# Optimization experiments

Measured on AMD Instinct MI355X. Metric: run time of the kernel, lower is better.

## Reference

```python
import jax, jax.numpy as jnp
import numpy as np

B, T, D, H = 4, 2048, 1024, 16
DK, DV, CHUNK = D // H, 2 * D // H, 64  # head_k_dim=64, head_v_dim=128 (expand_v=2.0)
EPS = 1e-5


def setup_inputs() -> dict:
    key = jax.random.key(0)
    ks = jax.random.split(key, 6)
    s = 0.02
    return {
        "x": jax.random.normal(ks[0], (B, T, D), jnp.float32),
        "Wq": jax.random.normal(ks[1], (D, H * DK), jnp.float32) * s,
        "Wk": jax.random.normal(ks[2], (D, H * DK), jnp.float32) * s,
        "Wv": jax.random.normal(ks[3], (D, H * DV), jnp.float32) * s,
        "Wg": jax.random.normal(ks[4], (D, H * DV), jnp.float32) * s,
        "Wo": jax.random.normal(ks[5], (H * DV, D), jnp.float32) * s,
        "g_norm_w": jnp.ones((DV,), jnp.float32),
    }


def _rope(q):
    # q: [B, T, H, DK]; non-interleaved (rotate-half) rotary, base 10000
    half = DK // 2
    inv_freq = 1.0 / (10000.0 ** (jnp.arange(half, dtype=jnp.float32) / half))
    freqs = jnp.arange(T, dtype=jnp.float32)[:, None] * inv_freq  # [T, half]
    cos = jnp.cos(freqs)[None, :, None, :]
    sin = jnp.sin(freqs)[None, :, None, :]
    q1, q2 = q[..., :half], q[..., half:]
    return jnp.concatenate([q1 * cos - q2 * sin, q2 * cos + q1 * sin], axis=-1)


def reference(x, Wq, Wk, Wv, Wg, Wo, g_norm_w):
    q = _rope((x @ Wq).reshape(B, T, H, DK)) * (DK ** -0.5)
    k = _rope((x @ Wk).reshape(B, T, H, DK))
    v = (x @ Wv).reshape(B, T, H, DV)

    N = T // CHUNK
    def tochunks(t):  # [B,T,H,Dh] -> [N,B,H,C,Dh]
        return t.reshape(B, N, CHUNK, H, t.shape[-1]).transpose(1, 0, 3, 2, 4)
    qc, kc, vc = tochunks(q), tochunks(k), tochunks(v)

    # per-head RetNet decay: gamma_h = 1 - 2^{-5-h}
    gamma = 1.0 - jnp.exp2(-5.0 - jnp.arange(H, dtype=jnp.float32))  # [H]
    i = jnp.arange(CHUNK, dtype=jnp.float32)
    # intra-chunk decay mask D[h,i,j] = gamma^{i-j} for j<=i else 0
    Dmask = jnp.where(i[:, None] >= i[None, :],
                      gamma[:, None, None] ** (i[:, None] - i[None, :]), 0.0)  # [H,C,C]
    cross = gamma[:, None] ** (i + 1.0)          # [H,C] query decay vs prev state
    kdec = gamma[:, None] ** (CHUNK - 1.0 - i)   # [H,C] key decay into new state
    chunk_dec = gamma ** CHUNK                   # [H]

    def step(S, qkv):
        q_, k_, v_ = qkv  # [B,H,C,DK], [B,H,C,DK], [B,H,C,DV]
        attn = jnp.einsum('bhid,bhjd->bhij', q_, k_) * Dmask
        o = jnp.einsum('bhij,bhjv->bhiv', attn, v_)
        o = o + jnp.einsum('bhid,bhdv->bhiv', q_ * cross[None, :, :, None], S)
        S = S * chunk_dec[None, :, None, None] + \
            jnp.einsum('bhjd,bhjv->bhdv', k_ * kdec[None, :, :, None], v_)
        return S, o

    S0 = jnp.zeros((B, H, DK, DV), x.dtype)
    _, o = jax.lax.scan(step, S0, (qc, kc, vc))  # [N,B,H,C,DV]
    o = o.transpose(1, 0, 3, 2, 4).reshape(B, T, H, DV)

    # fused RMSNorm + swish gate (FusedRMSNormSwishGate)
    g = (x @ Wg).reshape(B, T, H, DV)
    o = o * jax.lax.rsqrt(jnp.mean(o * o, axis=-1, keepdims=True) + EPS) * g_norm_w
    o = o * (g * jax.nn.sigmoid(g))
    return o.reshape(B, T, H * DV) @ Wo
```

## Files before the change

### kernel.cpp

```cpp
#include <hip/hip_runtime.h>
#include <hip/hip_bf16.h>
#include <math.h>

typedef unsigned short u16;
typedef unsigned int u32;
typedef __attribute__((ext_vector_type(8))) short bf16x8;
typedef __attribute__((ext_vector_type(4))) float f32x4;


__device__ __forceinline__ u16 f2bf(float f) {
  union { float f; unsigned u; } a; a.f = f;
  unsigned u = a.u;
  unsigned r = (u + 0x7fffu + ((u >> 16) & 1u)) >> 16;
  return (u16)r;
}
__device__ __forceinline__ float bf2f(u16 s) {
  union { unsigned u; float f; } a; a.u = ((unsigned)s) << 16; return a.f;
}

__global__ void k_sentinel(float* out) {
  if (threadIdx.x == 0 && blockIdx.x == 0) out[0] = 1.0e6f;
}

__device__ __forceinline__ void split8r(const float* t, bf16x8& hi, bf16x8& lo) {
#pragma unroll
  for (int m = 0; m < 8; ++m) {
    union { float f; u32 u; } c; c.f = t[m];
    union { u32 u; float f; } hf; hf.u = c.u & 0xffff0000u;
    union { float f; u32 u; } lw; lw.f = t[m] - hf.f;
    hi[m] = (short)(u16)(c.u >> 16);
    lo[m] = (short)(u16)(lw.u >> 16);
  }
}
__device__ __forceinline__ void split8p(const float* __restrict__ p, bf16x8& hi, bf16x8& lo) {
  f32x4 a = *(const f32x4*)p;
  f32x4 b = *(const f32x4*)(p + 4);
  float t[8];
  t[0]=a[0]; t[1]=a[1]; t[2]=a[2]; t[3]=a[3]; t[4]=b[0]; t[5]=b[1]; t[6]=b[2]; t[7]=b[3];
  split8r(t, hi, lo);
}

__device__ __forceinline__ void bar_lds() {
  asm volatile("s_waitcnt lgkmcnt(0)" ::: "memory");
  __builtin_amdgcn_sched_barrier(0);
  __builtin_amdgcn_s_barrier();
}

__device__ __forceinline__ void bar_vm() {
  asm volatile("s_waitcnt vmcnt(0)" ::: "memory");
  __builtin_amdgcn_sched_barrier(0);
  __builtin_amdgcn_s_barrier();
}

__device__ __forceinline__ void gload16(const u16* g, u16* l) {
  __builtin_amdgcn_global_load_lds(
      (const __attribute__((address_space(1))) unsigned int*)g,
      (__attribute__((address_space(3))) unsigned int*)l, 16, 0, 0);
}

__global__ __launch_bounds__(256) void k_cvt_x(const float* __restrict__ src, u16* __restrict__ dst) {
  int i = blockIdx.x * 256 + threadIdx.x;
  float4 v = ((const float4*)src)[i];
  ushort4 o;
  o.x = f2bf(v.x); o.y = f2bf(v.y); o.z = f2bf(v.z); o.w = f2bf(v.w);
  ((ushort4*)dst)[i] = o;
}

__global__ __launch_bounds__(256) void k_ropetab(float2* __restrict__ tab) {
  int idx = blockIdx.x * 256 + threadIdx.x;
  int t = idx >> 5, i = idx & 31;
  float invf = powf(10000.f, -(float)i * (1.f / 32.f));
  float ang = (float)t * invf;
  float2 cs; cs.x = cosf(ang); cs.y = sinf(ang);
  tab[idx] = cs;
}

__global__ __launch_bounds__(256) void k_transpose_all(
    const float* __restrict__ Wq, const float* __restrict__ Wk, const float* __restrict__ Wv,
    const float* __restrict__ Wg, const float* __restrict__ Wo,
    u16* __restrict__ Wqkb, u16* __restrict__ Wvgb, u16* __restrict__ Wob) {
  int z = blockIdx.x;
  const float* src; u16* dst; int K, N, bx, by;
  if (z < 1024)      { src = Wq; dst = Wqkb;                       K = 1024; N = 1024; int r = z;        bx = r & 31; by = r >> 5; }
  else if (z < 2048) { src = Wk; dst = Wqkb + (size_t)1024 * 1024; K = 1024; N = 1024; int r = z - 1024; bx = r & 31; by = r >> 5; }
  else if (z < 4096) { src = Wv; dst = Wvgb;                       K = 1024; N = 2048; int r = z - 2048; bx = r & 63; by = r >> 6; }
  else if (z < 6144) { src = Wg; dst = Wvgb + (size_t)2048 * 1024; K = 1024; N = 2048; int r = z - 4096; bx = r & 63; by = r >> 6; }
  else               { src = Wo; dst = Wob;                        K = 2048; N = 1024; int r = z - 6144; bx = r & 31; by = r >> 5; }
  __shared__ float tile[32][33];
  int n0 = bx * 32, k0 = by * 32;
  int tx = threadIdx.x & 31, ty = threadIdx.x >> 5;
  for (int r = 0; r < 32; r += 8)
    tile[ty + r][tx] = src[(size_t)(k0 + ty + r) * N + n0 + tx];
  __syncthreads();
  for (int r = 0; r < 32; r += 8)
    dst[(size_t)(n0 + ty + r) * K + k0 + tx] = f2bf(tile[tx][ty + r]);
}

#define STG64(t, sl)                                                                   \
  {                                                                                    \
    _Pragma("unroll")                                                                  \
    for (int kk = 0; kk < 2; ++kk) {                                                   \
      _Pragma("unroll")                                                                \
      for (int q = 0; q < 2; ++q) {                                                    \
        int s = w * 2 + q;                                                             \
        int dByte = s * 1024 + lane * 16;                                              \
        int u = dByte ^ (((dByte >> 9) & 1) << 5);                                     \
        int row = u >> 6, cb = u & 63;                                                 \
        gload16(&A[(size_t)(i0 + row) * K + (t) * 64 + kk * 32 + (cb >> 1)],           \
                &As[sl][kk][s * 512]);                                                 \
        gload16(&Bt[(size_t)(n0 + row) * K + (t) * 64 + kk * 32 + (cb >> 1)],          \
                &Bs[sl][kk][s * 512]);                                                 \
      }                                                                                \
    }                                                                                  \
  }

__global__ __launch_bounds__(256, 2) void k_gemm_qkvg(const u16* __restrict__ A, const u16* __restrict__ Bt,
                                                      float* __restrict__ qk, u16* __restrict__ vg,
                                                      const float2* __restrict__ tab, int K) {
  __shared__ __attribute__((aligned(16))) u16 As[2][2][128 * 32];
  __shared__ __attribute__((aligned(16))) u16 Bs[2][2][128 * 32];
  int id = blockIdx.y * 48 + blockIdx.x;
  int x = id & 7, loc = id >> 3;
  int bxg = loc / 48, rem = loc - bxg * 48;
  int by8 = rem / 6, bxi = rem - by8 * 6;
  int bx = bxg * 6 + bxi, by = x * 8 + by8;
  int i0 = by * 128, n0 = bx * 128;
  int tid = threadIdx.x;
  int lane = tid & 63, w = tid >> 6;
  int wr = (w >> 1) * 64, wc = (w & 1) * 64;
  f32x4 acc[4][4];
#pragma unroll
  for (int m = 0; m < 4; ++m)
#pragma unroll
    for (int n = 0; n < 4; ++n) acc[m][n] = (f32x4){0.f, 0.f, 0.f, 0.f};
  int fr = lane & 15, kq = lane >> 4;
  int nkt = K >> 6;

  STG64(0, 0);
  bar_vm();
  for (int t = 0; t < nkt; ++t) {
    int sl = t & 1;
    if (t + 1 < nkt) STG64(t + 1, sl ^ 1);
#pragma unroll
    for (int kk = 0; kk < 2; ++kk) {
      bf16x8 af[4], bfr[4];
#pragma unroll
      for (int m = 0; m < 4; ++m) {
        int rr = wr + m * 16 + fr;
        int idx = (rr * 32 + kq * 8) ^ (((rr >> 3) & 1) << 4);
        af[m] = *(const bf16x8*)&As[sl][kk][idx];
      }
#pragma unroll
      for (int n = 0; n < 4; ++n) {
        int rr = wc + n * 16 + fr;
        int idx = (rr * 32 + kq * 8) ^ (((rr >> 3) & 1) << 4);
        bfr[n] = *(const bf16x8*)&Bs[sl][kk][idx];
      }
      __builtin_amdgcn_s_setprio(1);
#pragma unroll
      for (int m = 0; m < 4; ++m)
#pragma unroll
        for (int n = 0; n < 4; ++n)
          acc[m][n] = __builtin_amdgcn_mfma_f32_16x16x32_bf16(af[m], bfr[n], acc[m][n], 0, 0, 0);
      __builtin_amdgcn_s_setprio(0);
    }
    bar_vm();
  }

  int rb = (lane >> 4) * 4, cb2 = lane & 15;
  if (n0 < 2048) {
    float scale = (n0 < 1024) ? 0.125f : 1.0f;
#pragma unroll
    for (int m = 0; m < 4; ++m)
#pragma unroll
      for (int n = 0; n < 2; ++n) {
        int gc = n0 + wc + n * 16 + cb2;
        int ii = n * 16 + cb2;
#pragma unroll
        for (int r = 0; r < 4; ++r) {
          int gr = i0 + wr + m * 16 + rb + r;
          int t = gr & 2047;
          float2 cs = tab[t * 32 + ii];
          float q1 = acc[m][n][r], q2 = acc[m][n + 2][r];
          qk[(size_t)gr * 2048 + gc]      = (q1 * cs.x - q2 * cs.y) * scale;
          qk[(size_t)gr * 2048 + gc + 32] = (q2 * cs.x + q1 * cs.y) * scale;
        }
      }
  } else {
#pragma unroll
    for (int m = 0; m < 4; ++m)
#pragma unroll
      for (int n = 0; n < 4; ++n) {
        int gr = i0 + wr + m * 16 + rb;
        int gc = n0 - 2048 + wc + n * 16 + cb2;
#pragma unroll
        for (int r = 0; r < 4; ++r)
          vg[(size_t)(gr + r) * 4096 + gc] = f2bf(acc[m][n][r]);
      }
  }
}

__global__ __launch_bounds__(256, 2) void k_gemm_out(const u16* __restrict__ A, const u16* __restrict__ Bt,
                                                     float* __restrict__ Cv, int N, int K) {
  __shared__ __attribute__((aligned(16))) u16 As[2][2][128 * 32];
  __shared__ __attribute__((aligned(16))) u16 Bs[2][2][128 * 32];
  int nbx = gridDim.x;
  int id = blockIdx.y * nbx + blockIdx.x;
  int cpx = (nbx * gridDim.y) >> 3;
  int sw = (id & 7) * cpx + (id >> 3);
  int bx = sw % nbx, by = sw / nbx;
  int i0 = by * 128, n0 = bx * 128;
  int tid = threadIdx.x;
  int lane = tid & 63, w = tid >> 6;
  int wr = (w >> 1) * 64, wc = (w & 1) * 64;
  f32x4 acc[4][4];
#pragma unroll
  for (int m = 0; m < 4; ++m)
#pragma unroll
    for (int n = 0; n < 4; ++n) acc[m][n] = (f32x4){0.f, 0.f, 0.f, 0.f};
  int fr = lane & 15, kq = lane >> 4;
  int nkt = K >> 6;

  STG64(0, 0);
  bar_vm();
  for (int t = 0; t < nkt; ++t) {
    int sl = t & 1;
    if (t + 1 < nkt) STG64(t + 1, sl ^ 1);
#pragma unroll
    for (int kk = 0; kk < 2; ++kk) {
      bf16x8 af[4], bfr[4];
#pragma unroll
      for (int m = 0; m < 4; ++m) {
        int rr = wr + m * 16 + fr;
        int idx = (rr * 32 + kq * 8) ^ (((rr >> 3) & 1) << 4);
        af[m] = *(const bf16x8*)&As[sl][kk][idx];
      }
#pragma unroll
      for (int n = 0; n < 4; ++n) {
        int rr = wc + n * 16 + fr;
        int idx = (rr * 32 + kq * 8) ^ (((rr >> 3) & 1) << 4);
        bfr[n] = *(const bf16x8*)&Bs[sl][kk][idx];
      }
      __builtin_amdgcn_s_setprio(1);
#pragma unroll
      for (int m = 0; m < 4; ++m)
#pragma unroll
        for (int n = 0; n < 4; ++n)
          acc[m][n] = __builtin_amdgcn_mfma_f32_16x16x32_bf16(af[m], bfr[n], acc[m][n], 0, 0, 0);
      __builtin_amdgcn_s_setprio(0);
    }
    bar_vm();
  }

  int rb = (lane >> 4) * 4, cb2 = lane & 15;
#pragma unroll
  for (int m = 0; m < 4; ++m)
#pragma unroll
    for (int n = 0; n < 4; ++n) {
      int gr = i0 + wr + m * 16 + rb;
      int gc = n0 + wc + n * 16 + cb2;
#pragma unroll
      for (int r = 0; r < 4; ++r)
        Cv[(size_t)(gr + r) * N + gc] = acc[m][n][r];
    }
}

__global__ __launch_bounds__(512) void k_retention(const float* __restrict__ qk, const u16* __restrict__ vg,
                                                   const float* __restrict__ gnw, u16* __restrict__ og) {
  int bh = blockIdx.x & 63, rq = blockIdx.x >> 6;
  int h = bh & 15, b = bh >> 4;
  int gi0 = rq * 16;

  __shared__ __attribute__((aligned(16))) float qs[16][68];
  __shared__ __attribute__((aligned(16))) float ks[64][68];
  __shared__ __attribute__((aligned(16))) u16 vst[128][88];
  __shared__ __attribute__((aligned(16))) u16 kta_h[8][520];
  __shared__ __attribute__((aligned(16))) u16 kta_l[8][520];
  __shared__ __attribute__((aligned(16))) u16 pa_h[16][68];
  __shared__ __attribute__((aligned(16))) u16 pa_l[16][68];
  __shared__ __attribute__((aligned(16))) u16 sst_h[8][1040];
  __shared__ __attribute__((aligned(16))) u16 sst_l[8][1040];
  __shared__ float dpow[72];
  __shared__ float ssred[8][16];

  int tid = threadIdx.x;
  int w = tid >> 6, l = tid & 63;
  int fr = l & 15, fq = l >> 4;
  float gamma = 1.f - exp2f(-5.f - (float)h);
  if (tid <= 64) dpow[tid] = powf(gamma, (float)tid);
  for (int c = tid; c < 4160; c += 512) { ((u32*)sst_h)[c] = 0; ((u32*)sst_l)[c] = 0; }
  __syncthreads();
  float cdec = dpow[64];

  int e0 = w * 16;
  float gww = gnw[e0 + fr];
  int khmax = (rq < 2) ? 1 : 2;

  int qi = tid >> 4, qd4 = (tid & 15) * 4;
  int sj = tid >> 3, sdg = (tid & 7) * 8;
  int vjp = tid & 31, ve8 = (tid >> 5) * 8;

  f32x4 Sacc[4][2];
#pragma unroll
  for (int dt = 0; dt < 4; ++dt)
#pragma unroll
    for (int nt = 0; nt < 2; ++nt) Sacc[dt][nt] = (f32x4){0.f, 0.f, 0.f, 0.f};

  f32x4 pq = (f32x4){0.f, 0.f, 0.f, 0.f};
  f32x4 pk0, pk1;
  bf16x8 pva, pvb;
  {
    int rowbase = b * 2048;
    if (tid < 256) pq = *(const f32x4*)&qk[(size_t)(rowbase + gi0 + qi) * 2048 + h * 64 + qd4];
    const float* kr = &qk[(size_t)(rowbase + sj) * 2048 + 1024 + h * 64 + sdg];
    pk0 = *(const f32x4*)kr;
    pk1 = *(const f32x4*)(kr + 4);
    const u16* vr = &vg[(size_t)(rowbase + 2 * vjp) * 4096 + h * 128 + ve8];
    pva = *(const bf16x8*)vr;
    pvb = *(const bf16x8*)(vr + 4096);
  }

  for (int n = 0; n < 32; ++n) {
    int rowbase = b * 2048 + n * 64;
    if (tid < 256) *(f32x4*)&qs[qi][qd4] = pq;
    {
      *(f32x4*)&ks[sj][sdg] = pk0;
      *(f32x4*)&ks[sj][sdg + 4] = pk1;
      float kdv = dpow[63 - sj];
      float kd[8];
#pragma unroll
      for (int m = 0; m < 4; ++m) { kd[m] = pk0[m] * kdv; kd[m + 4] = pk1[m] * kdv; }
      bf16x8 kh8, kl8;
      split8r(kd, kh8, kl8);
      int J = sj >> 3, s = sj & 7, dh = tid & 7;
#pragma unroll
      for (int m = 0; m < 8; ++m) {
        int blk = (dh * 8) | (m ^ dh);
        kta_h[J][blk * 8 + s] = (u16)kh8[m];
        kta_l[J][blk * 8 + s] = (u16)kl8[m];
      }
#pragma unroll
      for (int m = 0; m < 8; ++m)
        *(u32*)&vst[ve8 + m][2 * vjp] = (u32)(u16)pva[m] | ((u32)(u16)pvb[m] << 16);
    }
    __syncthreads();
    if (n < 31) {
      int rb2 = rowbase + 64;
      if (tid < 256) pq = *(const f32x4*)&qk[(size_t)(rb2 + gi0 + qi) * 2048 + h * 64 + qd4];
      const float* kr = &qk[(size_t)(rb2 + sj) * 2048 + 1024 + h * 64 + sdg];
      pk0 = *(const f32x4*)kr;
      pk1 = *(const f32x4*)(kr + 4);
      const u16* vr = &vg[(size_t)(rb2 + 2 * vjp) * 4096 + h * 128 + ve8];
      pva = *(const bf16x8*)vr;
      pvb = *(const bf16x8*)(vr + 4096);
    }
    bf16x8 qhc[2], qlc[2];
    split8p(&qs[fr][fq * 8], qhc[0], qlc[0]);
    split8p(&qs[fr][32 + fq * 8], qhc[1], qlc[1]);
    if (w < 4) {
      int ct = w;
      f32x4 at = (f32x4){0.f, 0.f, 0.f, 0.f};
      if (16 * ct <= gi0 + 15) {
#pragma unroll
        for (int kh = 0; kh < 2; ++kh) {
          bf16x8 kbh, kbl;
          split8p(&ks[16 * ct + fr][kh * 32 + fq * 8], kbh, kbl);
          at = __builtin_amdgcn_mfma_f32_16x16x32_bf16(kbh, qhc[kh], at, 0, 0, 0);
          at = __builtin_amdgcn_mfma_f32_16x16x32_bf16(kbl, qhc[kh], at, 0, 0, 0);
          at = __builtin_amdgcn_mfma_f32_16x16x32_bf16(kbh, qlc[kh], at, 0, 0, 0);
        }
      }
      int jb = 16 * ct + fq * 4;
      ushort4 wh, wl;
#pragma unroll
      for (int r = 0; r < 4; ++r) {
        int s = gi0 + fr - (jb + r);
        float val = (s >= 0) ? at[r] * dpow[s] : 0.f;
        union { float f; u32 u; } c; c.f = val;
        union { u32 u; float f; } hf; hf.u = c.u & 0xffff0000u;
        union { float f; u32 u; } lw; lw.f = val - hf.f;
        ((u16*)&wh)[r] = (u16)(c.u >> 16);
        ((u16*)&wl)[r] = (u16)(lw.u >> 16);
      }
      *(ushort4*)&pa_h[fr][jb] = wh;
      *(ushort4*)&pa_l[fr][jb] = wl;
    } else if (n < 31) {
      int eb = (w - 4) * 32;
#pragma unroll
      for (int dt = 0; dt < 4; ++dt)
#pragma unroll
        for (int nt = 0; nt < 2; ++nt)
#pragma unroll
          for (int r = 0; r < 4; ++r) Sacc[dt][nt][r] *= cdec;
      bf16x8 bv[2][2];
#pragma unroll
      for (int kh2 = 0; kh2 < 2; ++kh2)
#pragma unroll
        for (int nt = 0; nt < 2; ++nt)
          bv[kh2][nt] = *(const bf16x8*)&vst[eb + nt * 16 + fr][kh2 * 32 + fq * 8];
#pragma unroll
      for (int kh2 = 0; kh2 < 2; ++kh2) {
#pragma unroll
        for (int dt = 0; dt < 4; ++dt) {
          int d = dt * 16 + fr;
          int blk = d ^ ((dt * 2 + (fr >> 3)) & 7);
          bf16x8 ah = *(const bf16x8*)&kta_h[kh2 * 4 + fq][blk * 8];
          bf16x8 al = *(const bf16x8*)&kta_l[kh2 * 4 + fq][blk * 8];
#pragma unroll
          for (int nt = 0; nt < 2; ++nt) {
            Sacc[dt][nt] = __builtin_amdgcn_mfma_f32_16x16x32_bf16(ah, bv[kh2][nt], Sacc[dt][nt], 0, 0, 0);
            Sacc[dt][nt] = __builtin_amdgcn_mfma_f32_16x16x32_bf16(al, bv[kh2][nt], Sacc[dt][nt], 0, 0, 0);
          }
        }
      }
    }
    bar_lds();
    f32x4 o1 = (f32x4){0.f, 0.f, 0.f, 0.f};
    f32x4 o2 = (f32x4){0.f, 0.f, 0.f, 0.f};
#pragma unroll
    for (int kh2 = 0; kh2 < 2; ++kh2) {
      bf16x8 sh = *(const bf16x8*)&sst_h[kh2 * 4 + fq][(e0 + fr) * 8];
      bf16x8 sl = *(const bf16x8*)&sst_l[kh2 * 4 + fq][(e0 + fr) * 8];
      o2 = __builtin_amdgcn_mfma_f32_16x16x32_bf16(qhc[kh2], sh, o2, 0, 0, 0);
      o2 = __builtin_amdgcn_mfma_f32_16x16x32_bf16(qhc[kh2], sl, o2, 0, 0, 0);
      o2 = __builtin_amdgcn_mfma_f32_16x16x32_bf16(qlc[kh2], sh, o2, 0, 0, 0);
      if (kh2 < khmax) {
        bf16x8 ph = *(const bf16x8*)&pa_h[fr][kh2 * 32 + fq * 8];
        bf16x8 pl = *(const bf16x8*)&pa_l[fr][kh2 * 32 + fq * 8];
        bf16x8 bvv = *(const bf16x8*)&vst[e0 + fr][kh2 * 32 + fq * 8];
        o1 = __builtin_amdgcn_mfma_f32_16x16x32_bf16(ph, bvv, o1, 0, 0, 0);
        o1 = __builtin_amdgcn_mfma_f32_16x16x32_bf16(pl, bvv, o1, 0, 0, 0);
      }
    }
    float ofin[4], ssp[4];
#pragma unroll
    for (int r = 0; r < 4; ++r) {
      int gi = gi0 + fq * 4 + r;
      ofin[r] = o1[r] + dpow[gi + 1] * o2[r];
      ssp[r] = ofin[r] * ofin[r];
    }
#pragma unroll
    for (int r = 0; r < 4; ++r) {
      ssp[r] += __shfl_xor(ssp[r], 1, 64);
      ssp[r] += __shfl_xor(ssp[r], 2, 64);
      ssp[r] += __shfl_xor(ssp[r], 4, 64);
      ssp[r] += __shfl_xor(ssp[r], 8, 64);
    }
    if (fr == 0) {
#pragma unroll
      for (int r = 0; r < 4; ++r) ssred[w][fq * 4 + r] = ssp[r];
    }
    bar_lds();
#pragma unroll
    for (int r = 0; r < 4; ++r) {
      int i16 = fq * 4 + r;
      float tot = 0.f;
#pragma unroll
      for (int w2 = 0; w2 < 8; ++w2) tot += ssred[w2][i16];
      float rms = rsqrtf(tot * (1.f / 128.f) + 1e-5f);
      int grow = rowbase + gi0 + i16;
      float g = bf2f(vg[(size_t)grow * 4096 + 2048 + h * 128 + e0 + fr]);
      float y = ofin[r] * rms * gww * (g / (1.f + expf(-g)));
      og[(size_t)grow * 2048 + h * 128 + e0 + fr] = f2bf(y);
    }
    if (w >= 4 && n < 31) {
      int eb = (w - 4) * 32;
#pragma unroll
      for (int dt = 0; dt < 4; ++dt) {
        int g = dt * 2 + (fq >> 1);
#pragma unroll
        for (int nt = 0; nt < 2; ++nt) {
          int e = eb + nt * 16 + fr;
          ushort4 wh, wl;
#pragma unroll
          for (int r = 0; r < 4; ++r) {
            union { float f; u32 u; } c; c.f = Sacc[dt][nt][r];
            union { u32 u; float f; } hf; hf.u = c.u & 0xffff0000u;
            union { float f; u32 u; } lw; lw.f = Sacc[dt][nt][r] - hf.f;
            ((u16*)&wh)[r] = (u16)(c.u >> 16);
            ((u16*)&wl)[r] = (u16)(lw.u >> 16);
          }
          int idx = e * 8 + (fq & 1) * 4;
          *(ushort4*)&sst_h[g][idx] = wh;
          *(ushort4*)&sst_l[g][idx] = wl;
        }
      }
    }
  }
}

extern "C" void kernel_launch(void* const* d_in, const int* in_sizes, int n_in,
                              void* d_out, int out_size, void* d_ws, size_t ws_size,
                              hipStream_t stream) {
  const float* x   = (const float*)d_in[0];
  const float* Wq  = (const float*)d_in[1];
  const float* Wk  = (const float*)d_in[2];
  const float* Wv  = (const float*)d_in[3];
  const float* Wg  = (const float*)d_in[4];
  const float* Wo  = (const float*)d_in[5];
  const float* gnw = (const float*)d_in[6];
  float* out = (float*)d_out;

  const size_t MB = 1024 * 1024;
  char* ws = (char*)d_ws;
  u16*   xb   = (u16*)(ws + 0 * MB);
  u16*   Wqkb = (u16*)(ws + 16 * MB);
  u16*   Wvgb = (u16*)(ws + 20 * MB);
  float2* tab = (float2*)(ws + 28 * MB);
  float* qk   = (float*)(ws + 32 * MB);
  u16*   vg   = (u16*)(ws + 96 * MB);
  u16*   Wob  = (u16*)(ws + 160 * MB);
  u16*   og   = (u16*)(ws + 0 * MB);
  const size_t NEED = 164 * MB;
  if (ws_size < NEED) {
    k_sentinel<<<1, 64, 0, stream>>>(out);
    return;
  }

  k_cvt_x<<<8192, 256, 0, stream>>>(x, xb);
  k_ropetab<<<256, 256, 0, stream>>>(tab);
  k_transpose_all<<<8192, 256, 0, stream>>>(Wq, Wk, Wv, Wg, Wo, Wqkb, Wvgb, Wob);

  k_gemm_qkvg<<<dim3(48, 64), 256, 0, stream>>>(xb, Wqkb, qk, vg, tab, 1024);
  k_retention<<<256, 512, 0, stream>>>(qk, vg, gnw, og);
  k_gemm_out<<<dim3(8, 64), 256, 0, stream>>>(og, Wob, out, 1024, 2048);
}
```

Baseline: 288.9 us.

## Enlarge GEMM tiles to 256x128 with K-step 32 in both projection GEMMs

Measured after the change: 310.1 us. +7.3%, slower.

```diff
diff --git a/kernel.cpp b/kernel.cpp
--- a/kernel.cpp
+++ b/kernel.cpp
@@ -96,74 +96,73 @@
     dst[(size_t)(n0 + ty + r) * K + k0 + tx] = f2bf(tile[tx][ty + r]);
 }
 
-#define STG64(t, sl)                                                                   \
-  {                                                                                    \
-    _Pragma("unroll")                                                                  \
-    for (int kk = 0; kk < 2; ++kk) {                                                   \
-      _Pragma("unroll")                                                                \
-      for (int q = 0; q < 2; ++q) {                                                    \
-        int s = w * 2 + q;                                                             \
-        int dByte = s * 1024 + lane * 16;                                              \
-        int u = dByte ^ (((dByte >> 9) & 1) << 5);                                     \
-        int row = u >> 6, cb = u & 63;                                                 \
-        gload16(&A[(size_t)(i0 + row) * K + (t) * 64 + kk * 32 + (cb >> 1)],           \
-                &As[sl][kk][s * 512]);                                                 \
-        gload16(&Bt[(size_t)(n0 + row) * K + (t) * 64 + kk * 32 + (cb >> 1)],          \
-                &Bs[sl][kk][s * 512]);                                                 \
-      }                                                                                \
-    }                                                                                  \
+#define STG(t, sl)                                                                  \
+  {                                                                                 \
+    _Pragma("unroll")                                                               \
+    for (int q = 0; q < 4; ++q) {                                                   \
+      int s = w * 4 + q;                                                            \
+      int dByte = s * 1024 + lane * 16;                                             \
+      int u = dByte ^ (((dByte >> 9) & 1) << 5);                                    \
+      int row = u >> 6, cb = u & 63;                                                \
+      gload16(&A[(size_t)(i0 + row) * K + (t) * 32 + (cb >> 1)], &As[sl][s * 512]); \
+    }                                                                               \
+    _Pragma("unroll")                                                               \
+    for (int q = 0; q < 2; ++q) {                                                   \
+      int s = w * 2 + q;                                                            \
+      int dByte = s * 1024 + lane * 16;                                             \
+      int u = dByte ^ (((dByte >> 9) & 1) << 5);                                    \
+      int row = u >> 6, cb = u & 63;                                                \
+      gload16(&Bt[(size_t)(n0 + row) * K + (t) * 32 + (cb >> 1)], &Bs[sl][s * 512]);\
+    }                                                                               \
   }
 
 __global__ __launch_bounds__(256, 2) void k_gemm_qkvg(const u16* __restrict__ A, const u16* __restrict__ Bt,
                                                       float* __restrict__ qk, u16* __restrict__ vg,
                                                       const float2* __restrict__ tab, int K) {
-  __shared__ __attribute__((aligned(16))) u16 As[2][2][128 * 32];
-  __shared__ __attribute__((aligned(16))) u16 Bs[2][2][128 * 32];
-  int id = blockIdx.y * 48 + blockIdx.x;
-  int x = id & 7, loc = id >> 3;
-  int bxg = loc / 48, rem = loc - bxg * 48;
-  int by8 = rem / 6, bxi = rem - by8 * 6;
-  int bx = bxg * 6 + bxi, by = x * 8 + by8;
-  int i0 = by * 128, n0 = bx * 128;
+  __shared__ __attribute__((aligned(16))) u16 As[2][256 * 32];
+  __shared__ __attribute__((aligned(16))) u16 Bs[2][128 * 32];
+  int nbx = gridDim.x;
+  int id = blockIdx.y * nbx + blockIdx.x;
+  int cpx = (nbx * gridDim.y) >> 3;
+  int sw = (id & 7) * cpx + (id >> 3);
+  int bx = sw % nbx, by = sw / nbx;
+  int i0 = by * 256, n0 = bx * 128;
   int tid = threadIdx.x;
   int lane = tid & 63, w = tid >> 6;
-  int wr = (w >> 1) * 64, wc = (w & 1) * 64;
-  f32x4 acc[4][4];
-#pragma unroll
-  for (int m = 0; m < 4; ++m)
+  int wr = (w >> 1) * 128, wc = (w & 1) * 64;
+  f32x4 acc[8][4];
+#pragma unroll
+  for (int m = 0; m < 8; ++m)
 #pragma unroll
     for (int n = 0; n < 4; ++n) acc[m][n] = (f32x4){0.f, 0.f, 0.f, 0.f};
   int fr = lane & 15, kq = lane >> 4;
-  int nkt = K >> 6;
-
-  STG64(0, 0);
+  int nkt = K >> 5;
+
+  STG(0, 0);
   bar_vm();
   for (int t = 0; t < nkt; ++t) {
     int sl = t & 1;
-    if (t + 1 < nkt) STG64(t + 1, sl ^ 1);
-#pragma unroll
-    for (int kk = 0; kk < 2; ++kk) {
-      bf16x8 af[4], bfr[4];
-#pragma unroll
-      for (int m = 0; m < 4; ++m) {
-        int rr = wr + m * 16 + fr;
-        int idx = (rr * 32 + kq * 8) ^ (((rr >> 3) & 1) << 4);
-        af[m] = *(const bf16x8*)&As[sl][kk][idx];
-      }
-#pragma unroll
-      for (int n = 0; n < 4; ++n) {
-        int rr = wc + n * 16 + fr;
-        int idx = (rr * 32 + kq * 8) ^ (((rr >> 3) & 1) << 4);
-        bfr[n] = *(const bf16x8*)&Bs[sl][kk][idx];
-      }
-      __builtin_amdgcn_s_setprio(1);
-#pragma unroll
-      for (int m = 0; m < 4; ++m)
-#pragma unroll
-        for (int n = 0; n < 4; ++n)
-          acc[m][n] = __builtin_amdgcn_mfma_f32_16x16x32_bf16(af[m], bfr[n], acc[m][n], 0, 0, 0);
-      __builtin_amdgcn_s_setprio(0);
-    }
+    if (t + 1 < nkt) STG(t + 1, sl ^ 1);
+    bf16x8 af[8], bfr[4];
+#pragma unroll
+    for (int m = 0; m < 8; ++m) {
+      int rr = wr + m * 16 + fr;
+      int idx = (rr * 32 + kq * 8) ^ (((rr >> 3) & 1) << 4);
+      af[m] = *(const bf16x8*)&As[sl][idx];
+    }
+#pragma unroll
+    for (int n = 0; n < 4; ++n) {
+      int rr = wc + n * 16 + fr;
+      int idx = (rr * 32 + kq * 8) ^ (((rr >> 3) & 1) << 4);
+      bfr[n] = *(const bf16x8*)&Bs[sl][idx];
+    }
+    __builtin_amdgcn_s_setprio(1);
+#pragma unroll
+    for (int m = 0; m < 8; ++m)
+#pragma unroll
+      for (int n = 0; n < 4; ++n)
+        acc[m][n] = __builtin_amdgcn_mfma_f32_16x16x32_bf16(af[m], bfr[n], acc[m][n], 0, 0, 0);
+    __builtin_amdgcn_s_setprio(0);
     bar_vm();
   }
 
@@ -171,7 +170,7 @@
   if (n0 < 2048) {
     float scale = (n0 < 1024) ? 0.125f : 1.0f;
 #pragma unroll
-    for (int m = 0; m < 4; ++m)
+    for (int m = 0; m < 8; ++m)
 #pragma unroll
       for (int n = 0; n < 2; ++n) {
         int gc = n0 + wc + n * 16 + cb2;
@@ -188,7 +187,7 @@
       }
   } else {
 #pragma unroll
-    for (int m = 0; m < 4; ++m)
+    for (int m = 0; m < 8; ++m)
 #pragma unroll
       for (int n = 0; n < 4; ++n) {
         int gr = i0 + wr + m * 16 + rb;
@@ -202,59 +201,56 @@
 
 __global__ __launch_bounds__(256, 2) void k_gemm_out(const u16* __restrict__ A, const u16* __restrict__ Bt,
                                                      float* __restrict__ Cv, int N, int K) {
-  __shared__ __attribute__((aligned(16))) u16 As[2][2][128 * 32];
-  __shared__ __attribute__((aligned(16))) u16 Bs[2][2][128 * 32];
+  __shared__ __attribute__((aligned(16))) u16 As[2][256 * 32];
+  __shared__ __attribute__((aligned(16))) u16 Bs[2][128 * 32];
   int nbx = gridDim.x;
   int id = blockIdx.y * nbx + blockIdx.x;
   int cpx = (nbx * gridDim.y) >> 3;
   int sw = (id & 7) * cpx + (id >> 3);
   int bx = sw % nbx, by = sw / nbx;
-  int i0 = by * 128, n0 = bx * 128;
+  int i0 = by * 256, n0 = bx * 128;
   int tid = threadIdx.x;
   int lane = tid & 63, w = tid >> 6;
-  int wr = (w >> 1) * 64, wc = (w & 1) * 64;
-  f32x4 acc[4][4];
-#pragma unroll
-  for (int m = 0; m < 4; ++m)
+  int wr = (w >> 1) * 128, wc = (w & 1) * 64;
+  f32x4 acc[8][4];
+#pragma unroll
+  for (int m = 0; m < 8; ++m)
 #pragma unroll
     for (int n = 0; n < 4; ++n) acc[m][n] = (f32x4){0.f, 0.f, 0.f, 0.f};
   int fr = lane & 15, kq = lane >> 4;
-  int nkt = K >> 6;
-
-  STG64(0, 0);
+  int nkt = K >> 5;
+
+  STG(0, 0);
   bar_vm();
   for (int t = 0; t < nkt; ++t) {
     int sl = t & 1;
-    if (t + 1 < nkt) STG64(t + 1, sl ^ 1);
-#pragma unroll
-    for (int kk = 0; kk < 2; ++kk) {
-      bf16x8 af[4], bfr[4];
-#pragma unroll
-      for (int m = 0; m < 4; ++m) {
-        int rr = wr + m * 16 + fr;
-        int idx = (rr * 32 + kq * 8) ^ (((rr >> 3) & 1) << 4);
-        af[m] = *(const bf16x8*)&As[sl][kk][idx];
-      }
-#pragma unroll
-      for (int n = 0; n < 4; ++n) {
-        int rr = wc + n * 16 + fr;
-        int idx = (rr * 32 + kq * 8) ^ (((rr >> 3) & 1) << 4);
-        bfr[n] = *(const bf16x8*)&Bs[sl][kk][idx];
-      }
-      __builtin_amdgcn_s_setprio(1);
-#pragma unroll
-      for (int m = 0; m < 4; ++m)
-#pragma unroll
-        for (int n = 0; n < 4; ++n)
-          acc[m][n] = __builtin_amdgcn_mfma_f32_16x16x32_bf16(af[m], bfr[n], acc[m][n], 0, 0, 0);
-      __builtin_amdgcn_s_setprio(0);
-    }
+    if (t + 1 < nkt) STG(t + 1, sl ^ 1);
+    bf16x8 af[8], bfr[4];
+#pragma unroll
+    for (int m = 0; m < 8; ++m) {
+      int rr = wr + m * 16 + fr;
+      int idx = (rr * 32 + kq * 8) ^ (((rr >> 3) & 1) << 4);
+      af[m] = *(const bf16x8*)&As[sl][idx];
+    }
+#pragma unroll
+    for (int n = 0; n < 4; ++n) {
+      int rr = wc + n * 16 + fr;
+      int idx = (rr * 32 + kq * 8) ^ (((rr >> 3) & 1) << 4);
+      bfr[n] = *(const bf16x8*)&Bs[sl][idx];
+    }
+    __builtin_amdgcn_s_setprio(1);
+#pragma unroll
+    for (int m = 0; m < 8; ++m)
+#pragma unroll
+      for (int n = 0; n < 4; ++n)
+        acc[m][n] = __builtin_amdgcn_mfma_f32_16x16x32_bf16(af[m], bfr[n], acc[m][n], 0, 0, 0);
+    __builtin_amdgcn_s_setprio(0);
     bar_vm();
   }
 
   int rb = (lane >> 4) * 4, cb2 = lane & 15;
 #pragma unroll
-  for (int m = 0; m < 4; ++m)
+  for (int m = 0; m < 8; ++m)
 #pragma unroll
     for (int n = 0; n < 4; ++n) {
       int gr = i0 + wr + m * 16 + rb;
@@ -521,7 +517,7 @@
   k_ropetab<<<256, 256, 0, stream>>>(tab);
   k_transpose_all<<<8192, 256, 0, stream>>>(Wq, Wk, Wv, Wg, Wo, Wqkb, Wvgb, Wob);
 
-  k_gemm_qkvg<<<dim3(48, 64), 256, 0, stream>>>(xb, Wqkb, qk, vg, tab, 1024);
+  k_gemm_qkvg<<<dim3(48, 32), 256, 0, stream>>>(xb, Wqkb, qk, vg, tab, 1024);
   k_retention<<<256, 512, 0, stream>>>(qk, vg, gnw, og);
-  k_gemm_out<<<dim3(8, 64), 256, 0, stream>>>(og, Wob, out, 1024, 2048);
-}
+  k_gemm_out<<<dim3(8, 32), 256, 0, stream>>>(og, Wob, out, 1024, 2048);
+}
```
